# Kernel tuning notes

Hardware: AMD Instinct MI355X
Metric: run time of the kernel (lower is better)

The kernel has to match this reference:

```python
import jax, jax.numpy as jnp
import numpy as np

N_NODES = 50000
N_EDGES = 800000
IN_DIM, HID_DIM, OUT_DIM = 64, 128, 128


def _glorot(key, shape):
    fan_in, fan_out = shape[1], shape[0]
    lim = float(np.sqrt(6.0 / (fan_in + fan_out)))
    return jax.random.uniform(key, shape, jnp.float32, -lim, lim)


def setup_inputs() -> dict:
    key = jax.random.key(0)
    ks = jax.random.split(key, 8)
    x = jax.random.normal(ks[0], (N_NODES, IN_DIM), jnp.float32)
    edge_index = jax.random.randint(ks[1], (2, N_EDGES), 0, N_NODES, jnp.int64)
    return {
        "x": x,
        "edge_index": edge_index,
        # layer 1 (SAGEConv: lin_l acts on aggregated neighbors + bias, lin_r on root)
        "W1_l": _glorot(ks[2], (HID_DIM, IN_DIM)),
        "W1_r": _glorot(ks[3], (HID_DIM, IN_DIM)),
        "b1": jnp.zeros((HID_DIM,), jnp.float32),
        # layer 2
        "W2_l": _glorot(ks[4], (OUT_DIM, HID_DIM)),
        "W2_r": _glorot(ks[5], (OUT_DIM, HID_DIM)),
        "b2": jnp.zeros((OUT_DIM,), jnp.float32),
    }


def _sage_conv(x, src, dst, W_l, W_r, b):
    # mean aggregation of neighbor features: messages flow src -> dst
    msg = x[src]                                           # [E, D]
    agg = jax.ops.segment_sum(msg, dst, num_segments=N_NODES)  # [N, D]
    deg = jax.ops.segment_sum(jnp.ones((msg.shape[0],), x.dtype), dst,
                              num_segments=N_NODES)        # [N]
    mean = agg / jnp.maximum(deg, 1.0)[:, None]            # isolated nodes -> 0
    return mean @ W_l.T + x @ W_r.T + b


def reference(x, edge_index, W1_l, W1_r, b1, W2_l, W2_r, b2):
    src, dst = edge_index[0], edge_index[1]
    h = _sage_conv(x, src, dst, W1_l, W1_r, b1)
    h = jax.nn.relu(h)
    out = _sage_conv(h, src, dst, W2_l, W2_r, b2)
    return out
```

## Files before the change

kernel.cpp:

```cpp
#include <hip/hip_runtime.h>
#include <hip/hip_bf16.h>

constexpr int N  = 50000;
constexpr int E  = 800000;
constexpr int D0 = 64;
constexpr int D1 = 128;
constexpr int CAP = 64;

typedef __attribute__((ext_vector_type(8))) short short8;
typedef __attribute__((ext_vector_type(4))) float f32x4;

__device__ __forceinline__ unsigned short bf16bits(float f) {
    __hip_bfloat16 hb = __float2bfloat16(f);
    return *reinterpret_cast<unsigned short*>(&hb);
}

__device__ __forceinline__ void acc8(float* a, const uint4 r) {
    union { unsigned u; float f; } c;
    c.u = r.x << 16;         a[0] += c.f;
    c.u = r.x & 0xffff0000u; a[1] += c.f;
    c.u = r.y << 16;         a[2] += c.f;
    c.u = r.y & 0xffff0000u; a[3] += c.f;
    c.u = r.z << 16;         a[4] += c.f;
    c.u = r.z & 0xffff0000u; a[5] += c.f;
    c.u = r.w << 16;         a[6] += c.f;
    c.u = r.w & 0xffff0000u; a[7] += c.f;
}

__global__ void k_bin(const int* __restrict__ src, const int* __restrict__ dst,
                      int* __restrict__ cnt, int* __restrict__ bin) {
    int i = blockIdx.x * blockDim.x + threadIdx.x;
    int e0 = i * 4;
    if (e0 >= E) return;
    int4 d = *(const int4*)&dst[e0];
    int4 s = *(const int4*)&src[e0];
    int p0 = atomicAdd(&cnt[d.x], 1);
    int p1 = atomicAdd(&cnt[d.y], 1);
    int p2 = atomicAdd(&cnt[d.z], 1);
    int p3 = atomicAdd(&cnt[d.w], 1);
    if (p0 < CAP) bin[d.x * CAP + p0] = s.x;
    if (p1 < CAP) bin[d.y * CAP + p1] = s.y;
    if (p2 < CAP) bin[d.z * CAP + p2] = s.z;
    if (p3 < CAP) bin[d.w * CAP + p3] = s.w;
}

__global__ void k_cvtx(const float* __restrict__ x, unsigned short* __restrict__ xb) {
    int i = blockIdx.x * blockDim.x + threadIdx.x;
    if (i >= N * D0 / 8) return;
    const float4 v0 = *(const float4*)&x[(size_t)i * 8];
    const float4 v1 = *(const float4*)&x[(size_t)i * 8 + 4];
    float f[8] = {v0.x, v0.y, v0.z, v0.w, v1.x, v1.y, v1.z, v1.w};
    unsigned short u[8];
    #pragma unroll
    for (int j = 0; j < 8; ++j) u[j] = bf16bits(f[j]);
    *(short8*)&xb[(size_t)i * 8] = *(short8*)u;
}

__global__ void k_wprep(const float* __restrict__ W1l, const float* __restrict__ W1r,
                        const float* __restrict__ W2l, const float* __restrict__ W2r,
                        unsigned short* __restrict__ W1cat,
                        unsigned short* __restrict__ W2cat) {
    int i = blockIdx.x * blockDim.x + threadIdx.x;
    if (i < 128 * 128) {
        int o = i >> 7, k = i & 127;
        float v = (k < 64) ? W1l[o * 64 + k] : W1r[o * 64 + (k - 64)];
        W1cat[i] = bf16bits(v);
    }
    if (i < 128 * 256) {
        int o = i >> 8, k = i & 255;
        float v = (k < 128) ? W2l[o * 128 + k] : W2r[o * 128 + (k - 128)];
        W2cat[i] = bf16bits(v);
    }
}

template<int DIN>
__global__ __launch_bounds__(256, 8)
void k_gather(const unsigned short* __restrict__ xin,
              const int* __restrict__ cnt,
              const int* __restrict__ bin,
              unsigned short* __restrict__ mean) {
    constexpr int GRPSZ = DIN / 8;
    constexpr int GPB   = 256 / GRPSZ;
    const int tid      = threadIdx.x;
    const int sub      = tid & (GRPSZ - 1);
    const int gloc     = tid / GRPSZ;
    const int lane     = tid & 63;
    const int lanebase = (lane / GRPSZ) * GRPSZ;
    const int g0   = blockIdx.x * GPB + gloc;
    const int gstr = gridDim.x * GPB;

    for (int n = g0; n < N; n += gstr) {
        const int deg  = cnt[n];
        const int degc = min(deg, CAP);
        const int base = n * CAP;

        float a[8] = {0.f, 0.f, 0.f, 0.f, 0.f, 0.f, 0.f, 0.f};

        for (int b = 0; b < degc; b += GRPSZ) {
            int nb = (b + sub < degc) ? bin[base + b + sub] : 0;
            const int c = min(GRPSZ, degc - b);
            int j = 0;
            for (; j + 4 <= c; j += 4) {
                int s0 = __shfl(nb, lanebase + j + 0);
                int s1 = __shfl(nb, lanebase + j + 1);
                int s2 = __shfl(nb, lanebase + j + 2);
                int s3 = __shfl(nb, lanebase + j + 3);
                uint4 r0 = *(const uint4*)&xin[(size_t)s0 * DIN + sub * 8];
                uint4 r1 = *(const uint4*)&xin[(size_t)s1 * DIN + sub * 8];
                uint4 r2 = *(const uint4*)&xin[(size_t)s2 * DIN + sub * 8];
                uint4 r3 = *(const uint4*)&xin[(size_t)s3 * DIN + sub * 8];
                acc8(a, r0); acc8(a, r1); acc8(a, r2); acc8(a, r3);
            }
            for (; j < c; ++j) {
                int s = __shfl(nb, lanebase + j);
                uint4 r = *(const uint4*)&xin[(size_t)s * DIN + sub * 8];
                acc8(a, r);
            }
        }

        const float invd = 1.0f / fmaxf((float)deg, 1.0f);
        unsigned short u[8];
        #pragma unroll
        for (int q = 0; q < 8; ++q) u[q] = bf16bits(a[q] * invd);
        *(short8*)&mean[(size_t)n * DIN + sub * 8] = *(short8*)u;
    }
}

template<int DIN, bool RELU, bool OUT_BF16>
__global__ __launch_bounds__(256)
void k_mdense(const unsigned short* __restrict__ mean,
              const unsigned short* __restrict__ xin,
              const unsigned short* __restrict__ Wcat,
              const float* __restrict__ bias,
              void* __restrict__ out,
              int n_nodes) {
    constexpr int K  = 2 * DIN;
    constexpr int KP = K + 8;
    __shared__ unsigned short A[64 * KP];

    const int tid   = threadIdx.x;
    const int nbase = blockIdx.x * 64;

    constexpr int CPR   = K / 8;
    constexpr int TOTAL = 64 * CPR;
    for (int c = tid; c < TOTAL; c += 256) {
        int row  = c / CPR;
        int col8 = (c - row * CPR) * 8;
        int n    = nbase + row;
        short8 v = (short8)0;
        if (n < n_nodes) {
            const unsigned short* srcp = (col8 < DIN)
                ? &mean[(size_t)n * DIN + col8]
                : &xin[(size_t)n * DIN + (col8 - DIN)];
            v = *(const short8*)srcp;
        }
        *(short8*)&A[row * KP + col8] = v;
    }
    __syncthreads();

    const int lane = tid & 63;
    const int wv   = tid >> 6;
    const int l15  = lane & 15;
    const int kseg = lane >> 4;

    f32x4 acc[8];
    #pragma unroll
    for (int ot = 0; ot < 8; ++ot) acc[ot] = (f32x4){0.f, 0.f, 0.f, 0.f};

    #pragma unroll
    for (int kk = 0; kk < K / 32; ++kk) {
        short8 a = *(const short8*)&A[(wv * 16 + l15) * KP + kk * 32 + kseg * 8];
        #pragma unroll
        for (int ot = 0; ot < 8; ++ot) {
            short8 b = *(const short8*)&Wcat[(size_t)(ot * 16 + l15) * K + kk * 32 + kseg * 8];
            acc[ot] = __builtin_amdgcn_mfma_f32_16x16x32_bf16(a, b, acc[ot], 0, 0, 0);
        }
    }

    #pragma unroll
    for (int ot = 0; ot < 8; ++ot) {
        const int o  = ot * 16 + l15;
        const float bv = bias[o];
        #pragma unroll
        for (int i = 0; i < 4; ++i) {
            int n = nbase + wv * 16 + kseg * 4 + i;
            if (n < n_nodes) {
                float v = acc[ot][i] + bv;
                if constexpr (RELU) v = fmaxf(v, 0.0f);
                if constexpr (OUT_BF16) {
                    ((unsigned short*)out)[(size_t)n * 128 + o] = bf16bits(v);
                } else {
                    ((float*)out)[(size_t)n * 128 + o] = v;
                }
            }
        }
    }
}

extern "C" void kernel_launch(void* const* d_in, const int* in_sizes, int n_in,
                              void* d_out, int out_size, void* d_ws, size_t ws_size,
                              hipStream_t stream) {
    const float* x   = (const float*)d_in[0];
    const int*   ei  = (const int*)d_in[1];
    const float* W1l = (const float*)d_in[2];
    const float* W1r = (const float*)d_in[3];
    const float* b1  = (const float*)d_in[4];
    const float* W2l = (const float*)d_in[5];
    const float* W2r = (const float*)d_in[6];
    const float* b2  = (const float*)d_in[7];
    float*       out = (float*)d_out;

    const int* src = ei;
    const int* dst = ei + E;

    char* p = (char*)d_ws;
    auto alloc = [&](size_t bytes) -> char* {
        char* r = p; p += (bytes + 15) & ~(size_t)15; return r;
    };
    int*            cnt   = (int*)alloc(N * sizeof(int));
    int*            bin   = (int*)alloc((size_t)N * CAP * sizeof(int));
    unsigned short* xb    = (unsigned short*)alloc((size_t)N * D0 * 2);
    unsigned short* h     = (unsigned short*)alloc((size_t)N * D1 * 2);
    unsigned short* mean  = (unsigned short*)alloc((size_t)N * D1 * 2);
    unsigned short* W1cat = (unsigned short*)alloc(128 * 128 * 2);
    unsigned short* W2cat = (unsigned short*)alloc(128 * 256 * 2);

    const int nblk_d = (N + 63) / 64;

    k_cvtx<<<(N * D0 / 8 + 255) / 256, 256, 0, stream>>>(x, xb);
    k_wprep<<<(128 * 256 + 255) / 256, 256, 0, stream>>>(W1l, W1r, W2l, W2r, W1cat, W2cat);

    hipMemsetAsync(cnt, 0, (size_t)N * sizeof(int), stream);
    k_bin<<<(E / 4 + 255) / 256, 256, 0, stream>>>(src, dst, cnt, bin);

    k_gather<D0><<<2048, 256, 0, stream>>>(xb, cnt, bin, mean);
    k_mdense<D0, true, true>
        <<<nblk_d, 256, 0, stream>>>(mean, xb, W1cat, b1, h, N);

    k_gather<D1><<<2048, 256, 0, stream>>>(h, cnt, bin, mean);
    k_mdense<D1, false, false>
        <<<nblk_d, 256, 0, stream>>>(mean, h, W2cat, b2, out, N);
}
```

Measured before the change: 182.6 us.

## Partition edge binning by destination range across block groups

The binning kernel now launches NPART groups of blocks, and each group scans all edges but only inserts those whose destination falls in its node range. The aim is to localize atomic counter updates and bin writes into a smaller address window per group, so they hit better in cache (L2 / memory-side locality). In exchange, the edge arrays are read NPART times and more branch divergence is added.

```diff
diff --git a/kernel.cpp b/kernel.cpp
--- a/kernel.cpp
+++ b/kernel.cpp
@@ -6,6 +6,10 @@
 constexpr int D0 = 64;
 constexpr int D1 = 128;
 constexpr int CAP = 64;
+
+constexpr int NPART = 8;
+constexpr int PSZ   = (N + NPART - 1) / NPART;
+constexpr int BPP   = 128;
 
 typedef __attribute__((ext_vector_type(8))) short short8;
 typedef __attribute__((ext_vector_type(4))) float f32x4;
@@ -27,21 +31,35 @@
     c.u = r.w & 0xffff0000u; a[7] += c.f;
 }
 
-__global__ void k_bin(const int* __restrict__ src, const int* __restrict__ dst,
-                      int* __restrict__ cnt, int* __restrict__ bin) {
-    int i = blockIdx.x * blockDim.x + threadIdx.x;
-    int e0 = i * 4;
-    if (e0 >= E) return;
-    int4 d = *(const int4*)&dst[e0];
-    int4 s = *(const int4*)&src[e0];
-    int p0 = atomicAdd(&cnt[d.x], 1);
-    int p1 = atomicAdd(&cnt[d.y], 1);
-    int p2 = atomicAdd(&cnt[d.z], 1);
-    int p3 = atomicAdd(&cnt[d.w], 1);
-    if (p0 < CAP) bin[d.x * CAP + p0] = s.x;
-    if (p1 < CAP) bin[d.y * CAP + p1] = s.y;
-    if (p2 < CAP) bin[d.z * CAP + p2] = s.z;
-    if (p3 < CAP) bin[d.w * CAP + p3] = s.w;
+__global__ __launch_bounds__(256)
+void k_bin(const int* __restrict__ src, const int* __restrict__ dst,
+           int* __restrict__ cnt, int* __restrict__ bin) {
+    const int p     = blockIdx.x & (NPART - 1);
+    const int local = blockIdx.x >> 3;
+    const int lo = p * PSZ;
+    const int hi = min(N, lo + PSZ);
+
+    for (int i = local * 256 + threadIdx.x; i < E / 4; i += BPP * 256) {
+        const int e0 = i * 4;
+        int4 d = *(const int4*)&dst[e0];
+        int4 s = *(const int4*)&src[e0];
+        if (d.x >= lo && d.x < hi) {
+            int pos = atomicAdd(&cnt[d.x], 1);
+            if (pos < CAP) bin[d.x * CAP + pos] = s.x;
+        }
+        if (d.y >= lo && d.y < hi) {
+            int pos = atomicAdd(&cnt[d.y], 1);
+            if (pos < CAP) bin[d.y * CAP + pos] = s.y;
+        }
+        if (d.z >= lo && d.z < hi) {
+            int pos = atomicAdd(&cnt[d.z], 1);
+            if (pos < CAP) bin[d.z * CAP + pos] = s.z;
+        }
+        if (d.w >= lo && d.w < hi) {
+            int pos = atomicAdd(&cnt[d.w], 1);
+            if (pos < CAP) bin[d.w * CAP + pos] = s.w;
+        }
+    }
 }
 
 __global__ void k_cvtx(const float* __restrict__ x, unsigned short* __restrict__ xb) {
@@ -231,7 +249,7 @@
     k_wprep<<<(128 * 256 + 255) / 256, 256, 0, stream>>>(W1l, W1r, W2l, W2r, W1cat, W2cat);
 
     hipMemsetAsync(cnt, 0, (size_t)N * sizeof(int), stream);
-    k_bin<<<(E / 4 + 255) / 256, 256, 0, stream>>>(src, dst, cnt, bin);
+    k_bin<<<NPART * BPP, 256, 0, stream>>>(src, dst, cnt, bin);
 
     k_gather<D0><<<2048, 256, 0, stream>>>(xb, cnt, bin, mean);
     k_mdense<D0, true, true>
```

After: 173.1 us. 1.06x faster.
